# Performance work log

Measured on AMD Instinct MI355X. Metric: run time of the kernel, lower is better.

The kernel has to match this reference:

```python
import jax, jax.numpy as jnp
import numpy as np
from jax import lax

S, B, C = 128, 32, 16
VW, VC = 100000, 100
DW, DC = 256, 64
HW, HC = 512, 128
T = 17


def setup_inputs():
    key = jax.random.key(0)
    it = iter(jax.random.split(key, 40))

    def p(shape, scale=0.05):
        return jax.random.normal(next(it), shape, jnp.float32) * scale

    inp = {}
    inp['sentence'] = jax.random.randint(next(it), (S, B), 2, VW)
    inp['char'] = jax.random.randint(next(it), (B, S, C), 2, VC)
    inp['tags'] = jax.random.randint(next(it), (S, B), 0, T)
    inp['W_we'] = p((VW, DW)).at[1].set(0.0)  # padding_idx=1 row zeroed
    inp['W_ce'] = p((VC, DC)).at[1].set(0.0)
    Hc2, Hw2 = HC // 2, HW // 2
    for d in ('f', 'b'):
        inp['c_Wih_' + d] = p((4 * Hc2, DC))
        inp['c_Whh_' + d] = p((4 * Hc2, Hc2))
        inp['c_b_' + d] = p((4 * Hc2,))
        inp['w_Wih_' + d] = p((4 * Hw2, DW + HC))
        inp['w_Whh_' + d] = p((4 * Hw2, Hw2))
        inp['w_b_' + d] = p((4 * Hw2,))
    inp['emit_W'] = p((T, HW))
    inp['emit_b'] = p((T,))
    inp['crf_trans'] = p((T, T), 0.1)
    inp['crf_start'] = p((T,), 0.1)
    inp['crf_end'] = p((T,), 0.1)
    return inp


def _lstm(xs, Wih, Whh, b):
    # xs: (L, N, D); torch gate order i,f,g,o
    H = Whh.shape[1]

    def step(carry, x):
        h, c = carry
        g = x @ Wih.T + h @ Whh.T + b
        i, f, gg, o = jnp.split(g, 4, axis=-1)
        c = jax.nn.sigmoid(f) * c + jax.nn.sigmoid(i) * jnp.tanh(gg)
        h = jax.nn.sigmoid(o) * jnp.tanh(c)
        return (h, c), h

    z = jnp.zeros((xs.shape[1], H), xs.dtype)
    (hT, _), hs = lax.scan(step, (z, z), xs)
    return hs, hT


def _bilstm(xs, Wf, Uf, bf, Wb, Ub, bb):
    hs_f, hT_f = _lstm(xs, Wf, Uf, bf)
    hs_b, hT_b = _lstm(xs[::-1], Wb, Ub, bb)
    return jnp.concatenate([hs_f, hs_b[::-1]], axis=-1), hT_f, hT_b


def _crf_nll(em, tags, mask, trans, start, end):
    # em: (S,B,T); pytorch-crf log-likelihood, reduction='sum'; returns -llh
    b_idx = jnp.arange(em.shape[1])
    mf = mask.astype(em.dtype)
    score0 = start[tags[0]] + em[0, b_idx, tags[0]]

    def num_step(carry, inp):
        s, prev = carry
        e_t, t_t, m_t = inp
        s = s + (trans[prev, t_t] + e_t[b_idx, t_t]) * m_t
        prev = jnp.where(m_t > 0, t_t, prev)
        return (s, prev), None

    (num, last), _ = lax.scan(num_step, (score0, tags[0]), (em[1:], tags[1:], mf[1:]))
    num = num + end[last]

    alpha0 = start[None, :] + em[0]

    def den_step(alpha, inp):
        e_t, m_t = inp
        nxt = jax.scipy.special.logsumexp(alpha[:, :, None] + trans[None] + e_t[:, None, :], axis=1)
        return jnp.where(m_t[:, None] > 0, nxt, alpha), None

    alpha, _ = lax.scan(den_step, alpha0, (em[1:], mf[1:]))
    den = jax.scipy.special.logsumexp(alpha + end[None, :], axis=1)
    return -jnp.sum(num - den)


def reference(sentence, char, tags, W_we, W_ce, c_Wih_f, c_Whh_f, c_b_f, c_Wih_b, c_Whh_b, c_b_b, w_Wih_f, w_Whh_f, w_b_f, w_Wih_b, w_Whh_b, w_b_b, emit_W, emit_b, crf_trans, crf_start, crf_end):
    # char features: batch the per-position char BiLSTM across (B*S)
    ce = W_ce[char]  # (B,S,C,DC)
    ce = jnp.transpose(ce, (2, 0, 1, 3)).reshape(C, B * S, DC)
    _, hTf, hTb = _bilstm(ce, c_Wih_f, c_Whh_f, c_b_f, c_Wih_b, c_Whh_b, c_b_b)
    ch = jnp.concatenate([hTf, hTb], axis=-1).reshape(B, S, HC).transpose(1, 0, 2)  # (S,B,HC)
    x = jnp.concatenate([ch, W_we[sentence]], axis=-1)  # (S,B,HC+DW)
    out, _, _ = _bilstm(x, w_Wih_f, w_Whh_f, w_b_f, w_Wih_b, w_Whh_b, w_b_b)  # (S,B,HW)
    em = out @ emit_W.T + emit_b  # (S,B,T)
    mask = sentence != 1
    return _crf_nll(em, tags, mask, crf_trans, crf_start, crf_end)
```

## Files before the change

### kernel.cpp

```cpp
#include <hip/hip_runtime.h>
#include <math.h>

#define SS 128
#define BB 32
#define CC 16
#define DW 256
#define DC 64
#define HC 128
#define KX 384
#define TT 17

typedef __attribute__((ext_vector_type(8))) short bf16x8;
typedef __attribute__((ext_vector_type(4))) float f32x4;
typedef unsigned long long ull_t;

__device__ __forceinline__ float sigf(float x) { return 1.0f / (1.0f + __expf(-x)); }
__device__ __forceinline__ float tanhfast(float x) {
  float xc = fminf(fmaxf(x, -15.f), 15.f);
  float e = __expf(2.f * xc);
  return (e - 1.f) / (e + 1.f);
}
__device__ __forceinline__ unsigned short f2bf(float x) {
  unsigned int u = __float_as_uint(x);
  u += 0x7FFF + ((u >> 16) & 1);
  return (unsigned short)(u >> 16);
}
__device__ __forceinline__ unsigned ld_u32(const unsigned* p) {
  return __hip_atomic_load(p, __ATOMIC_RELAXED, __HIP_MEMORY_SCOPE_AGENT);
}
__device__ __forceinline__ void st_u32(unsigned* p, unsigned v) {
  __hip_atomic_store(p, v, __ATOMIC_RELAXED, __HIP_MEMORY_SCOPE_AGENT);
}
__device__ __forceinline__ ull_t ld_ull(const ull_t* p) {
  return __hip_atomic_load(p, __ATOMIC_RELAXED, __HIP_MEMORY_SCOPE_AGENT);
}
__device__ __forceinline__ void st_ull(ull_t* p, ull_t v) {
  __hip_atomic_store(p, v, __ATOMIC_RELAXED, __HIP_MEMORY_SCOPE_AGENT);
}

__global__ __launch_bounds__(256) void k0_ihvocab(
    const float* __restrict__ Wce,
    const float* __restrict__ WihF, const float* __restrict__ bF,
    const float* __restrict__ WihB, const float* __restrict__ bB,
    float* __restrict__ ihv) {
  int blk = blockIdx.x;
  int d = blk / 100, v = blk % 100;
  const float* Wih = d ? WihB : WihF;
  const float* bb  = d ? bB   : bF;
  __shared__ float ce[DC];
  if (threadIdx.x < DC) ce[threadIdx.x] = Wce[v * DC + threadIdx.x];
  __syncthreads();
  int g = threadIdx.x;
  float acc = bb[g];
  #pragma unroll 16
  for (int k = 0; k < DC; ++k) acc += ce[k] * Wih[g * DC + k];
  ihv[(d * 100 + v) * 256 + g] = acc;
}

__global__ __launch_bounds__(256) void k1_char(
    const int* __restrict__ charidx,
    const float* __restrict__ WhhF, const float* __restrict__ WhhB,
    const float* __restrict__ ihv,
    float* __restrict__ x)
{
  int blk = blockIdx.x;
  int d = blk >> 8;
  int n0 = (blk & 255) * 16;
  const float* Whh = d ? WhhB : WhhF;

  __shared__ float Wl[256 * 68];
  __shared__ float hl[16 * 68];

  for (int i = threadIdx.x; i < 256 * 64; i += 256) {
    int g = i >> 6, k = i & 63;
    Wl[g * 68 + k] = Whh[i];
  }
  __syncthreads();

  int hh = threadIdx.x & 63;
  int ng = threadIdx.x >> 6;
  float c[4] = {0.f, 0.f, 0.f, 0.f};
  float h[4] = {0.f, 0.f, 0.f, 0.f};
  int bb_[4], ss_[4];
  #pragma unroll
  for (int m = 0; m < 4; ++m) {
    int n = n0 + ng + 4 * m;
    bb_[m] = n >> 7; ss_[m] = n & 127;
  }

  for (int t = 0; t < CC; ++t) {
    int cpos = d ? (CC - 1 - t) : t;
    float acc[4][4];
    #pragma unroll
    for (int m = 0; m < 4; ++m) {
      int v = charidx[bb_[m] * (SS * CC) + ss_[m] * CC + cpos];
      const float* base = ihv + (d * 100 + v) * 256 + hh;
      acc[m][0] = base[0]; acc[m][1] = base[64]; acc[m][2] = base[128]; acc[m][3] = base[192];
    }
    if (t > 0) {
      #pragma unroll 4
      for (int k = 0; k < 64; k += 4) {
        float4 w4[4];
        #pragma unroll
        for (int q = 0; q < 4; ++q)
          w4[q] = *(const float4*)&Wl[(q * 64 + hh) * 68 + k];
        #pragma unroll
        for (int m = 0; m < 4; ++m) {
          float4 h4 = *(const float4*)&hl[(ng + 4 * m) * 68 + k];
          #pragma unroll
          for (int q = 0; q < 4; ++q)
            acc[m][q] += h4.x * w4[q].x + h4.y * w4[q].y + h4.z * w4[q].z + h4.w * w4[q].w;
        }
      }
      __syncthreads();
    }
    #pragma unroll
    for (int m = 0; m < 4; ++m) {
      float ig = sigf(acc[m][0]);
      float fg = sigf(acc[m][1]);
      float gg = tanhfast(acc[m][2]);
      float og = sigf(acc[m][3]);
      c[m] = fg * c[m] + ig * gg;
      h[m] = og * tanhfast(c[m]);
      hl[(ng + 4 * m) * 68 + hh] = h[m];
    }
    __syncthreads();
  }
  #pragma unroll
  for (int m = 0; m < 4; ++m) {
    int row = ss_[m] * BB + bb_[m];
    x[row * KX + d * 64 + hh] = h[m];
  }
}

__global__ __launch_bounds__(64) void k2_we(
    const int* __restrict__ sentence, const float* __restrict__ Wwe,
    float* __restrict__ x) {
  int row = blockIdx.x;
  int idx = sentence[row];
  const float4* src = (const float4*)(Wwe + (size_t)idx * DW);
  float4* dst = (float4*)(x + (size_t)row * KX + HC);
  dst[threadIdx.x] = src[threadIdx.x];
}

__global__ __launch_bounds__(256) void k3_ihgemm(
    const float* __restrict__ x,
    const float* __restrict__ WihF, const float* __restrict__ bF,
    const float* __restrict__ WihB, const float* __restrict__ bB,
    float* __restrict__ wg) {
  int n0 = blockIdx.x * 128;
  int m0 = blockIdx.y * 128;
  int d  = n0 >> 10;
  int gb = n0 & 1023;
  const float* Wih  = d ? WihB : WihF;
  const float* bias = d ? bB   : bF;

  __shared__ float At[32][132];
  __shared__ float Bt[32][132];

  int tid = threadIdx.x;
  int half = tid & 1, r = tid >> 1;
  int tm = tid & 15, tn = tid >> 4;
  float acc[8][8] = {};

  for (int k0 = 0; k0 < KX; k0 += 32) {
    __syncthreads();
    {
      const float4* srcA = (const float4*)(x + (size_t)(m0 + r) * KX + k0 + half * 16);
      const float4* srcB = (const float4*)(Wih + (size_t)(gb + r) * KX + k0 + half * 16);
      #pragma unroll
      for (int q = 0; q < 4; ++q) {
        float4 v = srcA[q];
        int kk = half * 16 + q * 4;
        At[kk + 0][r] = v.x; At[kk + 1][r] = v.y; At[kk + 2][r] = v.z; At[kk + 3][r] = v.w;
      }
      #pragma unroll
      for (int q = 0; q < 4; ++q) {
        float4 v = srcB[q];
        int kk = half * 16 + q * 4;
        Bt[kk + 0][r] = v.x; Bt[kk + 1][r] = v.y; Bt[kk + 2][r] = v.z; Bt[kk + 3][r] = v.w;
      }
    }
    __syncthreads();
    #pragma unroll 8
    for (int k = 0; k < 32; ++k) {
      float4 a0 = *(const float4*)&At[k][tm * 8];
      float4 a1 = *(const float4*)&At[k][tm * 8 + 4];
      float4 b0 = *(const float4*)&Bt[k][tn * 8];
      float4 b1 = *(const float4*)&Bt[k][tn * 8 + 4];
      float av[8] = {a0.x, a0.y, a0.z, a0.w, a1.x, a1.y, a1.z, a1.w};
      float bv[8] = {b0.x, b0.y, b0.z, b0.w, b1.x, b1.y, b1.z, b1.w};
      #pragma unroll
      for (int i = 0; i < 8; ++i)
        #pragma unroll
        for (int jq = 0; jq < 8; ++jq)
          acc[i][jq] += av[i] * bv[jq];
    }
  }
  float bv8[8];
  #pragma unroll
  for (int jq = 0; jq < 8; ++jq) bv8[jq] = bias[gb + tn * 8 + jq];
  #pragma unroll
  for (int i = 0; i < 8; ++i) {
    int m = m0 + tm * 8 + i;
    float* dst = wg + ((size_t)(d * 4096 + m)) * 1024 + gb + tn * 8;
    float4 v0 = {acc[i][0] + bv8[0], acc[i][1] + bv8[1], acc[i][2] + bv8[2], acc[i][3] + bv8[3]};
    float4 v1 = {acc[i][4] + bv8[4], acc[i][5] + bv8[5], acc[i][6] + bv8[6], acc[i][7] + bv8[7]};
    *(float4*)dst = v0; *(float4*)(dst + 4) = v1;
  }
}

__global__ __launch_bounds__(64, 1) void k4_word(
    const float* __restrict__ WhhF, const float* __restrict__ WhhB,
    const float* __restrict__ wg,
    float* __restrict__ outh,
    unsigned short* __restrict__ hbuf,
    unsigned int* __restrict__ flags) {
  const int blk = blockIdx.x;
  const int d = blk >> 4, widx = blk & 15;
  const int l = threadIdx.x;
  const int l15 = l & 15, q4 = l >> 4;
  const int j0w = widx * 16;
  const float* __restrict__ Whh = d ? WhhB : WhhF;
  unsigned short* hb_d = hbuf + d * 16384;
  unsigned int* fl = flags + d * 16;

  __shared__ unsigned short hl[32 * 24];

  bf16x8 Bf[4][8];
  #pragma unroll
  for (int q = 0; q < 4; ++q) {
    const float* wr = Whh + (size_t)(q * 256 + j0w + l15) * 256 + q4 * 8;
    #pragma unroll
    for (int ks = 0; ks < 8; ++ks) {
      float4 lo = *(const float4*)(wr + ks * 32);
      float4 hi = *(const float4*)(wr + ks * 32 + 4);
      bf16x8 f;
      f[0] = (short)f2bf(lo.x); f[1] = (short)f2bf(lo.y);
      f[2] = (short)f2bf(lo.z); f[3] = (short)f2bf(lo.w);
      f[4] = (short)f2bf(hi.x); f[5] = (short)f2bf(hi.y);
      f[6] = (short)f2bf(hi.z); f[7] = (short)f2bf(hi.w);
      Bf[q][ks] = f;
    }
  }

  float cst[8];
  #pragma unroll
  for (int i = 0; i < 8; ++i) cst[i] = 0.f;

  const int rb = l >> 1;
  const int rh = l & 1;

  for (int t = 0; t < SS; ++t) {
    const int s = d ? (SS - 1 - t) : t;

    f32x4 acc[4][2];
    const float* wgs = wg + ((size_t)d * 4096 + (size_t)s * 32) * 1024 + j0w + l15;
    #pragma unroll
    for (int q = 0; q < 4; ++q)
      #pragma unroll
      for (int mt = 0; mt < 2; ++mt)
        #pragma unroll
        for (int r = 0; r < 4; ++r)
          acc[q][mt][r] = wgs[(size_t)(q4 * 4 + r + mt * 16) * 1024 + q * 256];

    if (t > 0) {
      for (;;) {
        unsigned tg = ld_u32(fl + l15);
        if (__all((int)(tg >= (unsigned)t))) break;
        __builtin_amdgcn_s_sleep(1);
      }

      const unsigned short* hp = hb_d + ((t - 1) & 1) * 8192 + q4 * 8;
      bf16x8 Af[2][8];
      #pragma unroll
      for (int mt = 0; mt < 2; ++mt)
        #pragma unroll
        for (int ks = 0; ks < 8; ++ks) {
          const ull_t* p = (const ull_t*)(hp + (size_t)(l15 + mt * 16) * 256 + ks * 32);
          union { ull_t u[2]; bf16x8 v; } cvt;
          cvt.u[0] = ld_ull(p);
          cvt.u[1] = ld_ull(p + 1);
          Af[mt][ks] = cvt.v;
        }
      #pragma unroll
      for (int q = 0; q < 4; ++q)
        #pragma unroll
        for (int mt = 0; mt < 2; ++mt) {
          f32x4 c = acc[q][mt];
          #pragma unroll
          for (int ks = 0; ks < 8; ++ks)
            c = __builtin_amdgcn_mfma_f32_16x16x32_bf16(Af[mt][ks], Bf[q][ks], c, 0, 0, 0);
          acc[q][mt] = c;
        }
    }

    float hv[8];
    #pragma unroll
    for (int mt = 0; mt < 2; ++mt)
      #pragma unroll
      for (int r = 0; r < 4; ++r) {
        int ix = mt * 4 + r;
        float ig = sigf(acc[0][mt][r]);
        float fg = sigf(acc[1][mt][r]);
        float gg = tanhfast(acc[2][mt][r]);
        float og = sigf(acc[3][mt][r]);
        float c2 = fg * cst[ix] + ig * gg;
        cst[ix] = c2;
        hv[ix] = og * tanhfast(c2);
      }

    #pragma unroll
    for (int mt = 0; mt < 2; ++mt)
      #pragma unroll
      for (int r = 0; r < 4; ++r)
        hl[(q4 * 4 + r + mt * 16) * 24 + l15] = f2bf(hv[mt * 4 + r]);
    ull_t plo = *(const ull_t*)&hl[rb * 24 + rh * 8];
    ull_t phi = *(const ull_t*)&hl[rb * 24 + rh * 8 + 4];
    ull_t* dst = (ull_t*)(hb_d + (t & 1) * 8192 + (size_t)rb * 256 + j0w + rh * 8);
    st_ull(dst, plo);
    st_ull(dst + 1, phi);
    asm volatile("s_waitcnt vmcnt(0)" ::: "memory");
    if (l == 0) st_u32(fl + widx, (unsigned)(t + 1));

    float* op = outh + (size_t)(s * 32) * 512 + d * 256 + j0w + l15;
    #pragma unroll
    for (int mt = 0; mt < 2; ++mt)
      #pragma unroll
      for (int r = 0; r < 4; ++r)
        __builtin_nontemporal_store(hv[mt * 4 + r], op + (size_t)(q4 * 4 + r + mt * 16) * 512);
  }
}

__global__ __launch_bounds__(64) void k5_emit(
    const float* __restrict__ outh, const float* __restrict__ eW,
    const float* __restrict__ eb, float* __restrict__ em) {
  int row = blockIdx.x;
  int t = threadIdx.x;
  if (t < TT) {
    const float4* o4 = (const float4*)(outh + (size_t)row * 512);
    const float4* w4 = (const float4*)(eW + (size_t)t * 512);
    float acc = 0.f;
    #pragma unroll 16
    for (int k = 0; k < 128; ++k) {
      float4 a = o4[k], bq = w4[k];
      acc += a.x * bq.x + a.y * bq.y + a.z * bq.z + a.w * bq.w;
    }
    em[row * TT + t] = acc + eb[t];
  }
}

__global__ __launch_bounds__(64) void k6_crf(
    const int* __restrict__ sentence, const int* __restrict__ tags,
    const float* __restrict__ em, const float* __restrict__ trans,
    const float* __restrict__ startv, const float* __restrict__ endv,
    float* __restrict__ outp) {
  int b = blockIdx.x;
  int j = threadIdx.x;
  __shared__ float ash[TT];
  __shared__ float red[TT];
  float tc[TT];
  float alpha = 0.f;
  if (j < TT) {
    #pragma unroll
    for (int i = 0; i < TT; ++i) tc[i] = trans[i * TT + j];
    alpha = startv[j] + em[(0 * BB + b) * TT + j];
  }
  for (int s = 1; s < SS; ++s) {
    if (j < TT) ash[j] = alpha;
    __syncthreads();
    int m = (sentence[s * BB + b] != 1) ? 1 : 0;
    if (j < TT) {
      float mx = -1e30f;
      #pragma unroll
      for (int i = 0; i < TT; ++i) mx = fmaxf(mx, ash[i] + tc[i]);
      float sum = 0.f;
      #pragma unroll
      for (int i = 0; i < TT; ++i) sum += __expf(ash[i] + tc[i] - mx);
      float nxt = mx + __logf(sum) + em[(s * BB + b) * TT + j];
      if (m) alpha = nxt;
    }
    __syncthreads();
  }
  if (j < TT) red[j] = alpha + endv[j];
  __syncthreads();
  if (j == 0) {
    float mx = -1e30f;
    for (int i = 0; i < TT; ++i) mx = fmaxf(mx, red[i]);
    float sum = 0.f;
    for (int i = 0; i < TT; ++i) sum += __expf(red[i] - mx);
    float den = mx + __logf(sum);
    int prev = tags[0 * BB + b];
    float num = startv[prev] + em[(0 * BB + b) * TT + prev];
    for (int s = 1; s < SS; ++s) {
      int tg = tags[s * BB + b];
      if (sentence[s * BB + b] != 1) {
        num += trans[prev * TT + tg] + em[(s * BB + b) * TT + tg];
        prev = tg;
      }
    }
    num += endv[prev];
    atomicAdd(outp, den - num);
  }
}

extern "C" void kernel_launch(void* const* d_in, const int* in_sizes, int n_in,
                              void* d_out, int out_size, void* d_ws, size_t ws_size,
                              hipStream_t stream) {
  (void)in_sizes; (void)n_in; (void)out_size; (void)ws_size;
  const int*   sentence = (const int*)d_in[0];
  const int*   charidx  = (const int*)d_in[1];
  const int*   tags     = (const int*)d_in[2];
  const float* Wwe   = (const float*)d_in[3];
  const float* Wce   = (const float*)d_in[4];
  const float* cWihF = (const float*)d_in[5];
  const float* cWhhF = (const float*)d_in[6];
  const float* cbF   = (const float*)d_in[7];
  const float* wWihF = (const float*)d_in[8];
  const float* wWhhF = (const float*)d_in[9];
  const float* wbF   = (const float*)d_in[10];
  const float* cWihB = (const float*)d_in[11];
  const float* cWhhB = (const float*)d_in[12];
  const float* cbB   = (const float*)d_in[13];
  const float* wWihB = (const float*)d_in[14];
  const float* wWhhB = (const float*)d_in[15];
  const float* wbB   = (const float*)d_in[16];
  const float* eW    = (const float*)d_in[17];
  const float* eb    = (const float*)d_in[18];
  const float* trans = (const float*)d_in[19];
  const float* startv= (const float*)d_in[20];
  const float* endv  = (const float*)d_in[21];

  char* ws = (char*)d_ws;
  unsigned int*   flags = (unsigned int*)(ws + 0);
  float*          ihv   = (float*)(ws + 512);
  float*          x     = (float*)(ws + 205312);
  float*          wg    = (float*)(ws + 6496768);
  unsigned short* hbuf  = (unsigned short*)(ws + 40051200);
  float*          outh  = (float*)(ws + 40116736);
  float*          em    = (float*)(ws + 48505344);

  hipMemsetAsync(flags, 0, 512, stream);
  hipMemsetAsync(d_out, 0, sizeof(float), stream);

  k0_ihvocab<<<200, 256, 0, stream>>>(Wce, cWihF, cbF, cWihB, cbB, ihv);
  k1_char<<<512, 256, 0, stream>>>(charidx, cWhhF, cWhhB, ihv, x);
  k2_we<<<4096, 64, 0, stream>>>(sentence, Wwe, x);
  k3_ihgemm<<<dim3(16, 32), 256, 0, stream>>>(x, wWihF, wbF, wWihB, wbB, wg);
  k4_word<<<32, 64, 0, stream>>>(wWhhF, wWhhB, wg, outh, hbuf, flags);
  k5_emit<<<4096, 64, 0, stream>>>(outh, eW, eb, em);
  k6_crf<<<32, 64, 0, stream>>>(sentence, tags, em, trans, startv, endv, (float*)d_out);
}
```

Before: 1.010 ms.

## Co-locate word LSTM workgroups on one XCD and sync via XCD-local cache

The word BiLSTM kernel now launches 256 workgroups. Each one reads its XCC_ID and takes a ticket, and the first XCD to collect 32 workgroups wins. The other workgroups exit, so all the recurrent workers share one L2. Hidden-state exchange and step flags then use sc0 loads and stores that stay XCD-local, with agent-scope copies kept as a fallback path if polling times out. It also drops nontemporal stores on outh and packs 3 rows per block in the emission kernel. The trade-off is extra duplicate stores per step and a dependence on XCD scheduling and cache coherence behaviour.

```diff
diff --git a/kernel.cpp b/kernel.cpp
--- a/kernel.cpp
+++ b/kernel.cpp
@@ -12,6 +12,7 @@
 
 typedef __attribute__((ext_vector_type(8))) short bf16x8;
 typedef __attribute__((ext_vector_type(4))) float f32x4;
+typedef __attribute__((ext_vector_type(4))) unsigned int u32x4;
 typedef unsigned long long ull_t;
 
 __device__ __forceinline__ float sigf(float x) { return 1.0f / (1.0f + __expf(-x)); }
@@ -25,6 +26,9 @@
   u += 0x7FFF + ((u >> 16) & 1);
   return (unsigned short)(u >> 16);
 }
+__device__ __forceinline__ bf16x8 as_bf16x8(u32x4 v) {
+  union { u32x4 u; bf16x8 b; } c; c.u = v; return c.b;
+}
 __device__ __forceinline__ unsigned ld_u32(const unsigned* p) {
   return __hip_atomic_load(p, __ATOMIC_RELAXED, __HIP_MEMORY_SCOPE_AGENT);
 }
@@ -37,6 +41,21 @@
 __device__ __forceinline__ void st_ull(ull_t* p, ull_t v) {
   __hip_atomic_store(p, v, __ATOMIC_RELAXED, __HIP_MEMORY_SCOPE_AGENT);
 }
+
+#define LD8_SC0(A0,A1,A2,A3,A4,A5,A6,A7,PTR)                                  \
+  asm volatile(                                                               \
+    "global_load_dwordx4 %0, %8, off sc0\n\t"                                 \
+    "global_load_dwordx4 %1, %8, off offset:64 sc0\n\t"                       \
+    "global_load_dwordx4 %2, %8, off offset:128 sc0\n\t"                      \
+    "global_load_dwordx4 %3, %8, off offset:192 sc0\n\t"                      \
+    "global_load_dwordx4 %4, %8, off offset:256 sc0\n\t"                      \
+    "global_load_dwordx4 %5, %8, off offset:320 sc0\n\t"                      \
+    "global_load_dwordx4 %6, %8, off offset:384 sc0\n\t"                      \
+    "global_load_dwordx4 %7, %8, off offset:448 sc0\n\t"                      \
+    "s_waitcnt vmcnt(0)"                                                      \
+    : "=v"(A0), "=v"(A1), "=v"(A2), "=v"(A3),                                 \
+      "=v"(A4), "=v"(A5), "=v"(A6), "=v"(A7)                                  \
+    : "v"(PTR) : "memory")
 
 __global__ __launch_bounds__(256) void k0_ihvocab(
     const float* __restrict__ Wce,
@@ -215,15 +234,39 @@
     const float* __restrict__ wg,
     float* __restrict__ outh,
     unsigned short* __restrict__ hbuf,
-    unsigned int* __restrict__ flags) {
-  const int blk = blockIdx.x;
-  const int d = blk >> 4, widx = blk & 15;
+    unsigned short* __restrict__ hbuf2,
+    unsigned int* __restrict__ ctrl) {
   const int l = threadIdx.x;
+
+  unsigned xcd;
+  asm volatile("s_getreg_b32 %0, hwreg(HW_REG_XCC_ID)" : "=s"(xcd));
+  xcd &= 7u;
+  unsigned ticket = 0xffffffffu;
+  if (l == 0) {
+    ticket = atomicAdd(&ctrl[xcd], 1u);
+    if (ticket == 31u) atomicCAS(&ctrl[8], 0u, xcd + 1u);
+  }
+  ticket = (unsigned)__shfl((int)ticket, 0);
+  unsigned win = 0u;
+  for (int it = 0; it < (1 << 20); ++it) {
+    win = ld_u32(&ctrl[8]);
+    if (win != 0u) break;
+    __builtin_amdgcn_s_sleep(2);
+  }
+  if (win == 0u || xcd + 1u != win || ticket >= 32u) return;
+
+  const int d = (int)(ticket >> 4), widx = (int)(ticket & 15u);
   const int l15 = l & 15, q4 = l >> 4;
   const int j0w = widx * 16;
   const float* __restrict__ Whh = d ? WhhB : WhhF;
-  unsigned short* hb_d = hbuf + d * 16384;
-  unsigned int* fl = flags + d * 16;
+  unsigned short* hb_d  = hbuf  + d * 16384;
+  unsigned short* hb2_d = hbuf2 + d * 16384;
+  unsigned int* ftag = ctrl + 256  + d * 256;
+  unsigned int* stag = ctrl + 1024 + d * 256;
+  unsigned int* myftag = ftag + widx * 16;
+  unsigned int* mystag = stag + widx * 16;
+  const unsigned int* pollf = ftag + l15 * 16;
+  const unsigned int* polls = stag + l15 * 16;
 
   __shared__ unsigned short hl[32 * 24];
 
@@ -250,6 +293,7 @@
 
   const int rb = l >> 1;
   const int rh = l & 1;
+  int slow = 0;
 
   for (int t = 0; t < SS; ++t) {
     const int s = d ? (SS - 1 - t) : t;
@@ -265,24 +309,51 @@
           acc[q][mt][r] = wgs[(size_t)(q4 * 4 + r + mt * 16) * 1024 + q * 256];
 
     if (t > 0) {
-      for (;;) {
-        unsigned tg = ld_u32(fl + l15);
-        if (__all((int)(tg >= (unsigned)t))) break;
-        __builtin_amdgcn_s_sleep(1);
-      }
-
-      const unsigned short* hp = hb_d + ((t - 1) & 1) * 8192 + q4 * 8;
+      if (!slow) {
+        int ok = 0;
+        for (int it = 0; it < 16384; ++it) {
+          unsigned tg;
+          asm volatile("global_load_dword %0, %1, off sc0\n\ts_waitcnt vmcnt(0)"
+                       : "=v"(tg) : "v"((const void*)pollf) : "memory");
+          if (__all((int)(tg >= (unsigned)t))) { ok = 1; break; }
+        }
+        if (!ok) slow = 1;
+      }
+      if (slow) {
+        for (int it = 0; it < (1 << 20); ++it) {
+          unsigned tg = ld_u32(polls);
+          if (__all((int)(tg >= (unsigned)t))) break;
+          __builtin_amdgcn_s_sleep(1);
+        }
+      }
+
       bf16x8 Af[2][8];
-      #pragma unroll
-      for (int mt = 0; mt < 2; ++mt)
-        #pragma unroll
-        for (int ks = 0; ks < 8; ++ks) {
-          const ull_t* p = (const ull_t*)(hp + (size_t)(l15 + mt * 16) * 256 + ks * 32);
-          union { ull_t u[2]; bf16x8 v; } cvt;
-          cvt.u[0] = ld_ull(p);
-          cvt.u[1] = ld_ull(p + 1);
-          Af[mt][ks] = cvt.v;
+      if (!slow) {
+        #pragma unroll
+        for (int mt = 0; mt < 2; ++mt) {
+          const unsigned short* hp =
+              hb_d + ((t - 1) & 1) * 8192 + (size_t)(l15 + mt * 16) * 256 + q4 * 8;
+          u32x4 a0, a1, a2, a3, a4, a5, a6, a7;
+          LD8_SC0(a0, a1, a2, a3, a4, a5, a6, a7, (const void*)hp);
+          Af[mt][0] = as_bf16x8(a0); Af[mt][1] = as_bf16x8(a1);
+          Af[mt][2] = as_bf16x8(a2); Af[mt][3] = as_bf16x8(a3);
+          Af[mt][4] = as_bf16x8(a4); Af[mt][5] = as_bf16x8(a5);
+          Af[mt][6] = as_bf16x8(a6); Af[mt][7] = as_bf16x8(a7);
         }
+      } else {
+        const unsigned short* hp2 = hb2_d + ((t - 1) & 1) * 8192 + q4 * 8;
+        #pragma unroll
+        for (int mt = 0; mt < 2; ++mt)
+          #pragma unroll
+          for (int ks = 0; ks < 8; ++ks) {
+            const ull_t* p = (const ull_t*)(hp2 + (size_t)(l15 + mt * 16) * 256 + ks * 32);
+            union { ull_t u[2]; bf16x8 v; } cvt;
+            cvt.u[0] = ld_ull(p);
+            cvt.u[1] = ld_ull(p + 1);
+            Af[mt][ks] = cvt.v;
+          }
+      }
+
       #pragma unroll
       for (int q = 0; q < 4; ++q)
         #pragma unroll
@@ -315,38 +386,47 @@
       #pragma unroll
       for (int r = 0; r < 4; ++r)
         hl[(q4 * 4 + r + mt * 16) * 24 + l15] = f2bf(hv[mt * 4 + r]);
-    ull_t plo = *(const ull_t*)&hl[rb * 24 + rh * 8];
-    ull_t phi = *(const ull_t*)&hl[rb * 24 + rh * 8 + 4];
-    ull_t* dst = (ull_t*)(hb_d + (t & 1) * 8192 + (size_t)rb * 256 + j0w + rh * 8);
-    st_ull(dst, plo);
-    st_ull(dst + 1, phi);
+    u32x4 pdata = *(const u32x4*)&hl[rb * 24 + rh * 8];
+    {
+      void* dstf = (void*)(hb_d + (t & 1) * 8192 + (size_t)rb * 256 + j0w + rh * 8);
+      asm volatile("global_store_dwordx4 %0, %1, off sc0" :: "v"(dstf), "v"(pdata) : "memory");
+      ull_t* dsts = (ull_t*)(hb2_d + (t & 1) * 8192 + (size_t)rb * 256 + j0w + rh * 8);
+      union { u32x4 u; ull_t q[2]; } pu; pu.u = pdata;
+      st_ull(dsts, pu.q[0]);
+      st_ull(dsts + 1, pu.q[1]);
+    }
     asm volatile("s_waitcnt vmcnt(0)" ::: "memory");
-    if (l == 0) st_u32(fl + widx, (unsigned)(t + 1));
+    if (l == 0) {
+      asm volatile("global_store_dword %0, %1, off sc0"
+                   :: "v"((void*)myftag), "v"((unsigned)(t + 1)) : "memory");
+      st_u32(mystag, (unsigned)(t + 1));
+    }
 
     float* op = outh + (size_t)(s * 32) * 512 + d * 256 + j0w + l15;
     #pragma unroll
     for (int mt = 0; mt < 2; ++mt)
       #pragma unroll
       for (int r = 0; r < 4; ++r)
-        __builtin_nontemporal_store(hv[mt * 4 + r], op + (size_t)(q4 * 4 + r + mt * 16) * 512);
+        op[(size_t)(q4 * 4 + r + mt * 16) * 512] = hv[mt * 4 + r];
   }
 }
 
 __global__ __launch_bounds__(64) void k5_emit(
     const float* __restrict__ outh, const float* __restrict__ eW,
     const float* __restrict__ eb, float* __restrict__ em) {
-  int row = blockIdx.x;
   int t = threadIdx.x;
-  if (t < TT) {
+  int rr = t / 17, tt = t % 17;
+  int row = blockIdx.x * 3 + rr;
+  if (rr < 3 && row < 4096) {
     const float4* o4 = (const float4*)(outh + (size_t)row * 512);
-    const float4* w4 = (const float4*)(eW + (size_t)t * 512);
+    const float4* w4 = (const float4*)(eW + (size_t)tt * 512);
     float acc = 0.f;
     #pragma unroll 16
     for (int k = 0; k < 128; ++k) {
       float4 a = o4[k], bq = w4[k];
       acc += a.x * bq.x + a.y * bq.y + a.z * bq.z + a.w * bq.w;
     }
-    em[row * TT + t] = acc + eb[t];
+    em[row * TT + tt] = acc + eb[tt];
   }
 }
 
@@ -432,22 +512,23 @@
   const float* endv  = (const float*)d_in[21];
 
   char* ws = (char*)d_ws;
-  unsigned int*   flags = (unsigned int*)(ws + 0);
-  float*          ihv   = (float*)(ws + 512);
-  float*          x     = (float*)(ws + 205312);
-  float*          wg    = (float*)(ws + 6496768);
-  unsigned short* hbuf  = (unsigned short*)(ws + 40051200);
-  float*          outh  = (float*)(ws + 40116736);
-  float*          em    = (float*)(ws + 48505344);
-
-  hipMemsetAsync(flags, 0, 512, stream);
+  unsigned int*   ctrl  = (unsigned int*)(ws + 0);
+  float*          ihv   = (float*)(ws + 8192);
+  float*          x     = (float*)(ws + 212992);
+  float*          wg    = (float*)(ws + 6504448);
+  unsigned short* hbuf  = (unsigned short*)(ws + 40058880);
+  unsigned short* hbuf2 = (unsigned short*)(ws + 40124416);
+  float*          outh  = (float*)(ws + 40189952);
+  float*          em    = (float*)(ws + 48578560);
+
+  hipMemsetAsync(ctrl, 0, 8192, stream);
   hipMemsetAsync(d_out, 0, sizeof(float), stream);
 
   k0_ihvocab<<<200, 256, 0, stream>>>(Wce, cWihF, cbF, cWihB, cbB, ihv);
   k1_char<<<512, 256, 0, stream>>>(charidx, cWhhF, cWhhB, ihv, x);
   k2_we<<<4096, 64, 0, stream>>>(sentence, Wwe, x);
   k3_ihgemm<<<dim3(16, 32), 256, 0, stream>>>(x, wWihF, wbF, wWihB, wbB, wg);
-  k4_word<<<32, 64, 0, stream>>>(wWhhF, wWhhB, wg, outh, hbuf, flags);
-  k5_emit<<<4096, 64, 0, stream>>>(outh, eW, eb, em);
+  k4_word<<<256, 64, 0, stream>>>(wWhhF, wWhhB, wg, outh, hbuf, hbuf2, ctrl);
+  k5_emit<<<1366, 64, 0, stream>>>(outh, eW, eb, em);
   k6_crf<<<32, 64, 0, stream>>>(sentence, tags, em, trans, startv, endv, (float*)d_out);
 }
```

Result: slower. 2.766 ms (+173.7%).
